# Kernel optimization log

Hardware: AMD Instinct MI355X
Metric: run time of the kernel (lower is better)

Reference implementation:

```python
import jax, jax.numpy as jnp
import numpy as np

D_IN = 1024
D_OUT = 1024
NUM_HEADS = 16
HEAD_DIM = D_OUT // NUM_HEADS


def setup_inputs() -> dict:
    key = jax.random.key(0)
    k_x, k_q, k_k, k_v, k_o, k_ob = jax.random.split(key, 6)
    s_in = 1.0 / np.sqrt(D_IN)
    s_out = 1.0 / np.sqrt(D_OUT)
    return {
        "x": jax.random.normal(k_x, (2, 2048, D_IN), dtype=jnp.float32),
        "W_q": jax.random.uniform(k_q, (D_IN, D_OUT), minval=-s_in, maxval=s_in, dtype=jnp.float32),
        "W_k": jax.random.uniform(k_k, (D_IN, D_OUT), minval=-s_in, maxval=s_in, dtype=jnp.float32),
        "W_v": jax.random.uniform(k_v, (D_IN, D_OUT), minval=-s_in, maxval=s_in, dtype=jnp.float32),
        "W_out": jax.random.uniform(k_o, (D_OUT, D_OUT), minval=-s_out, maxval=s_out, dtype=jnp.float32),
        "b_out": jax.random.uniform(k_ob, (D_OUT,), minval=-s_out, maxval=s_out, dtype=jnp.float32),
    }


def reference(x, W_q, W_k, W_v, W_out, b_out):
    b, t, _ = x.shape
    # projections (qkv_bias=False)
    q = (x @ W_q).reshape(b, t, NUM_HEADS, HEAD_DIM).transpose(0, 2, 1, 3)  # [b,h,t,d]
    k = (x @ W_k).reshape(b, t, NUM_HEADS, HEAD_DIM).transpose(0, 2, 1, 3)
    v = (x @ W_v).reshape(b, t, NUM_HEADS, HEAD_DIM).transpose(0, 2, 1, 3)
    scale = 1.0 / np.sqrt(HEAD_DIM).astype(np.float32)
    scores = jnp.einsum("bhqd,bhkd->bhqk", q, k) * scale  # [b,h,t,t]
    causal = jnp.triu(jnp.ones((t, t), dtype=bool), k=1)
    scores = jnp.where(causal, -jnp.inf, scores)
    weights = jax.nn.softmax(scores, axis=-1)
    # dropout p=0.0 -> identity
    context = jnp.einsum("bhqk,bhkd->bhqd", weights, v)
    context = context.transpose(0, 2, 1, 3).reshape(b, t, D_OUT)
    return context @ W_out + b_out
```

## Files before the change

kernel.cpp:

```cpp
#include <hip/hip_runtime.h>
#include <hip/hip_bf16.h>

#define B_  2
#define T_  2048
#define D_  1024
#define H_  16
#define DH_ 64
#define M_  (B_*T_)

typedef _Float16 f16;
typedef __attribute__((ext_vector_type(4))) _Float16 f16x4;
typedef __attribute__((ext_vector_type(8))) _Float16 f16x8;
typedef __attribute__((ext_vector_type(4))) float f32x4;

#define GLOAD_LDS(gp, lp) __builtin_amdgcn_global_load_lds( \
    (const __attribute__((address_space(1))) void*)(gp),    \
    (__attribute__((address_space(3))) void*)(lp), 16, 0, 0)

__global__ void prep(const float* __restrict__ x,
                     const float* __restrict__ wq, const float* __restrict__ wk,
                     const float* __restrict__ wv, const float* __restrict__ wo,
                     f16* __restrict__ xb, f16* __restrict__ wqkvT, f16* __restrict__ woutT) {
  __shared__ float tile[32][33];
  const int bid = blockIdx.x;
  if (bid < 2048) {
    size_t i = ((size_t)bid * 256 + threadIdx.x) * 8;
    float4 a = *(const float4*)(x + i);
    float4 b = *(const float4*)(x + i + 4);
    f16x8 o;
    o[0]=(f16)a.x; o[1]=(f16)a.y; o[2]=(f16)a.z; o[3]=(f16)a.w;
    o[4]=(f16)b.x; o[5]=(f16)b.y; o[6]=(f16)b.z; o[7]=(f16)b.w;
    *(f16x8*)(xb + i) = o;
  } else {
    const int b2 = bid - 2048;
    const int j = b2 >> 10, rem = b2 & 1023;
    const float* src = (j==0)?wq:(j==1)?wk:(j==2)?wv:wo;
    f16* dst = (j<3) ? (wqkvT + (size_t)j*D_*D_) : woutT;
    const int n0 = (rem & 31)*32, k0 = (rem >> 5)*32;
    const int tx = threadIdx.x & 31, ty = threadIdx.x >> 5;
    #pragma unroll
    for (int i=0;i<32;i+=8)
      tile[ty+i][tx] = src[(size_t)(k0+ty+i)*D_ + n0+tx];
    __syncthreads();
    #pragma unroll
    for (int i=0;i<32;i+=8)
      dst[(size_t)(n0+ty+i)*D_ + k0+tx] = (f16)tile[tx][ty+i];
  }
}

__launch_bounds__(256, 2)
__global__ void qkv_gemm(const f16* __restrict__ xb, const f16* __restrict__ wT,
                         f16* __restrict__ Qp, f16* __restrict__ Kp, f16* __restrict__ Vtp) {
  const int fid = blockIdx.x;
  const int g = fid & 7, r = fid >> 3;
  const int m0 = ((((r & 3) << 3) | g)) * 128;
  const int n0 = ((r >> 2) & 7) * 128;
  const int j  = r >> 5;
  const f16* B0 = wT + (size_t)j * D_ * D_;
  __shared__ alignas(16) char smem[65536];
  f16* AsF = (f16*)smem;
  f16* BsF = AsF + 2*128*64;
  const int tid = threadIdx.x;
  const int lane = tid & 63, wave = tid >> 6;
  const int ln = lane & 15, quad = lane >> 4;
  const int wm = wave >> 1, wn = wave & 1;

  f32x4 acc[4][4];
  #pragma unroll
  for (int a=0;a<4;++a)
    #pragma unroll
    for (int b=0;b<4;++b) acc[a][b] = f32x4{0.f,0.f,0.f,0.f};

  const bool swapped = (j < 2);
  const int slot_row[4] = { (0*256+tid)>>3, (1*256+tid)>>3, (2*256+tid)>>3, (3*256+tid)>>3 };

  #pragma unroll
  for (int p = 0; p < 4; ++p) {
    int slot = p*256 + tid;
    int row  = slot_row[p];
    int c    = (slot & 7) ^ (row & 7);
    GLOAD_LDS(xb + (size_t)(m0+row)*D_ + c*8, AsF + (size_t)slot*8);
    GLOAD_LDS(B0 + (size_t)(n0+row)*D_ + c*8, BsF + (size_t)slot*8);
  }
  __syncthreads();

  for (int it = 0; it < 16; ++it) {
    const f16* Ac = AsF + (it & 1)*8192;
    const f16* Bc = BsF + (it & 1)*8192;
    if (it < 15) {
      const int k1 = (it + 1) * 64;
      f16* An = AsF + ((it + 1) & 1)*8192;
      f16* Bn = BsF + ((it + 1) & 1)*8192;
      #pragma unroll
      for (int p = 0; p < 4; ++p) {
        int slot = p*256 + tid;
        int row  = slot_row[p];
        int c    = (slot & 7) ^ (row & 7);
        GLOAD_LDS(xb + (size_t)(m0+row)*D_ + k1 + c*8, An + (size_t)slot*8);
        GLOAD_LDS(B0 + (size_t)(n0+row)*D_ + k1 + c*8, Bn + (size_t)slot*8);
      }
    }
    #pragma unroll
    for (int ks = 0; ks < 2; ++ks) {
      const int cb = ((ks*4 + quad) ^ (ln & 7)) * 8;
      f16x8 af[4], bf[4];
      #pragma unroll
      for (int mt = 0; mt < 4; ++mt)
        af[mt] = *(const f16x8*)(Ac + (size_t)(wm*64 + mt*16 + ln)*64 + cb);
      #pragma unroll
      for (int nt = 0; nt < 4; ++nt)
        bf[nt] = *(const f16x8*)(Bc + (size_t)(wn*64 + nt*16 + ln)*64 + cb);
      if (swapped) {
        #pragma unroll
        for (int nt = 0; nt < 4; ++nt)
          #pragma unroll
          for (int mt = 0; mt < 4; ++mt)
            acc[nt][mt] = __builtin_amdgcn_mfma_f32_16x16x32_f16(bf[nt], af[mt], acc[nt][mt], 0, 0, 0);
      } else {
        #pragma unroll
        for (int mt = 0; mt < 4; ++mt)
          #pragma unroll
          for (int nt = 0; nt < 4; ++nt)
            acc[mt][nt] = __builtin_amdgcn_mfma_f32_16x16x32_f16(af[mt], bf[nt], acc[mt][nt], 0, 0, 0);
      }
    }
    __syncthreads();
  }

  if (swapped) {
    const float scale = (j == 0) ? 0.125f : 1.0f;
    f16* dstB = (j == 0) ? Qp : Kp;
    #pragma unroll
    for (int nt = 0; nt < 4; ++nt)
      #pragma unroll
      for (int mt = 0; mt < 4; ++mt) {
        int gm = m0 + wm*64 + mt*16 + ln;
        int gn = n0 + wn*64 + nt*16 + quad*4;
        int bb = gm >> 11, t = gm & (T_-1);
        int h  = gn >> 6,  dd = gn & (DH_-1);
        f16x4 v;
        #pragma unroll
        for (int rr = 0; rr < 4; ++rr) v[rr] = (f16)(acc[nt][mt][rr] * scale);
        *(f16x4*)&dstB[((((size_t)bb*H_ + h)*T_ + t)*DH_) + dd] = v;
      }
  } else {
    f16* VtS = (f16*)smem;
    #pragma unroll
    for (int mt = 0; mt < 4; ++mt)
      #pragma unroll
      for (int nt = 0; nt < 4; ++nt) {
        f16x4 v;
        v[0]=(f16)acc[mt][nt][0]; v[1]=(f16)acc[mt][nt][1];
        v[2]=(f16)acc[mt][nt][2]; v[3]=(f16)acc[mt][nt][3];
        *(f16x4*)&VtS[(size_t)(wn*64 + nt*16 + ln)*136 + wm*64 + mt*16 + quad*4] = v;
      }
    __syncthreads();
    int dd_loc = tid >> 1, half = tid & 1;
    int gn = n0 + dd_loc, h = gn >> 6, dd = gn & (DH_-1);
    int bb = m0 >> 11, tb = (m0 & (T_-1)) + half*64;
    f16* dst = Vtp + ((size_t)(bb*H_ + h)*DH_ + dd)*T_ + tb;
    const f16* src = VtS + (size_t)dd_loc*136 + half*64;
    #pragma unroll
    for (int u = 0; u < 8; ++u)
      *(uint4*)(dst + u*8) = *(const uint4*)(src + u*8);
  }
}

__launch_bounds__(256, 3)
__global__ void flash(const f16* __restrict__ Qp, const f16* __restrict__ Kp,
                      const f16* __restrict__ Vtp, f16* __restrict__ ctx) {
  const int fid = blockIdx.x;
  const int bh = fid & 31;
  const int qt = 31 - (fid >> 5);
  const int b = bh >> 4, h = bh & (H_-1);
  const f16* Kh = Kp  + (size_t)bh * T_ * DH_;
  const f16* Vh = Vtp + (size_t)bh * DH_ * T_;
  const f16* Qh = Qp  + (size_t)bh * T_ * DH_;
  const int tid = threadIdx.x, lane = tid & 63, w = tid >> 6;
  const int ln = lane & 15, quad = lane >> 4;
  __shared__ alignas(16) f16 Ks[2*64*64];
  __shared__ alignas(16) f16 Vs[2*64*64];
  __shared__ alignas(16) f16 Ps[64][72];

  const int qw = qt*64 + w*16;

  f16x8 qf[2];
  #pragma unroll
  for (int ks = 0; ks < 2; ++ks)
    qf[ks] = *(const f16x8*)&Qh[(size_t)(qw + ln)*DH_ + ks*32 + quad*8];

  f32x4 o[4];
  #pragma unroll
  for (int dt = 0; dt < 4; ++dt) o[dt] = f32x4{0.f,0.f,0.f,0.f};
  float l_part = 0.f;

  #pragma unroll
  for (int i = 0; i < 2; ++i) {
    int row = w*16 + i*8 + (lane >> 3);
    int c   = (lane & 7) ^ (row & 7);
    GLOAD_LDS(Kh + (size_t)row*DH_ + c*8, Ks + (w*128 + i*64 + lane)*8);
    GLOAD_LDS(Vh + (size_t)row*T_  + c*8, Vs + (w*128 + i*64 + lane)*8);
  }
  __syncthreads();

  for (int it = 0; it <= qt; ++it) {
    const f16* Kc = Ks + (it & 1)*4096;
    const f16* Vc = Vs + (it & 1)*4096;
    if (it < qt) {
      const int kv1 = (it + 1)*64;
      f16* Kn = Ks + ((it + 1) & 1)*4096;
      f16* Vn = Vs + ((it + 1) & 1)*4096;
      #pragma unroll
      for (int i = 0; i < 2; ++i) {
        int row = w*16 + i*8 + (lane >> 3);
        int c   = (lane & 7) ^ (row & 7);
        GLOAD_LDS(Kh + (size_t)(kv1 + row)*DH_ + c*8, Kn + (w*128 + i*64 + lane)*8);
        GLOAD_LDS(Vh + (size_t)row*T_ + kv1 + c*8,    Vn + (w*128 + i*64 + lane)*8);
      }
    }

    f32x4 s[4];
    #pragma unroll
    for (int kt = 0; kt < 4; ++kt) s[kt] = f32x4{0.f,0.f,0.f,0.f};
    #pragma unroll
    for (int ks = 0; ks < 2; ++ks) {
      f16x8 kx[4];
      #pragma unroll
      for (int kt = 0; kt < 4; ++kt)
        kx[kt] = *(const f16x8*)(Kc + (size_t)(kt*16 + ln)*64 + (((ks*4 + quad) ^ (ln & 7))*8));
      #pragma unroll
      for (int kt = 0; kt < 4; ++kt)
        s[kt] = __builtin_amdgcn_mfma_f32_16x16x32_f16(kx[kt], qf[ks], s[kt], 0, 0, 0);
    }
    if (it == qt) {
      const int kv0 = it*64;
      #pragma unroll
      for (int kt = 0; kt < 4; ++kt)
        #pragma unroll
        for (int rr = 0; rr < 4; ++rr)
          if (kv0 + kt*16 + quad*4 + rr > qw + ln) s[kt][rr] = -INFINITY;
    }
    #pragma unroll
    for (int kt = 0; kt < 4; ++kt) {
      f16x4 pk;
      #pragma unroll
      for (int rr = 0; rr < 4; ++rr) {
        float pe = __expf(s[kt][rr]);
        l_part += pe;
        pk[rr] = (f16)pe;
      }
      *(f16x4*)&Ps[w*16 + ln][kt*16 + quad*4] = pk;
    }
    asm volatile("" ::: "memory");

    #pragma unroll
    for (int ks = 0; ks < 2; ++ks) {
      f16x8 px = *(const f16x8*)&Ps[w*16 + ln][ks*32 + quad*8];
      #pragma unroll
      for (int dt = 0; dt < 4; ++dt) {
        f16x8 vy = *(const f16x8*)(Vc + (size_t)(dt*16 + ln)*64 + (((ks*4 + quad) ^ (ln & 7))*8));
        o[dt] = __builtin_amdgcn_mfma_f32_16x16x32_f16(px, vy, o[dt], 0, 0, 0);
      }
    }
    __syncthreads();
  }

  float l = l_part;
  l += __shfl_xor(l, 16, 64);
  l += __shfl_xor(l, 32, 64);
  float inv = 1.0f / l;
  #pragma unroll
  for (int rr = 0; rr < 4; ++rr) {
    float linv = __shfl(inv, quad*4 + rr, 64);
    int t = qt*64 + w*16 + quad*4 + rr;
    #pragma unroll
    for (int dt = 0; dt < 4; ++dt)
      ctx[(size_t)(b*T_ + t)*D_ + h*DH_ + dt*16 + ln] = (f16)(o[dt][rr] * linv);
  }
}

__launch_bounds__(256, 2)
__global__ void out_gemm(const f16* __restrict__ ctx, const f16* __restrict__ woT,
                         const float* __restrict__ bo, float* __restrict__ out) {
  const int fid = blockIdx.x;
  const int g = fid & 7, r = fid >> 3;
  const int m0 = ((((r & 3) << 3) | g)) * 128;
  const int n0 = (r >> 2) * 128;
  __shared__ alignas(16) f16 smem[4*128*64];
  f16* AsF = smem;
  f16* BsF = AsF + 2*128*64;
  const int tid = threadIdx.x;
  const int lane = tid & 63, wave = tid >> 6;
  const int ln = lane & 15, quad = lane >> 4;
  const int wm = wave >> 1, wn = wave & 1;

  f32x4 acc[4][4];
  #pragma unroll
  for (int a=0;a<4;++a)
    #pragma unroll
    for (int b=0;b<4;++b) acc[a][b] = f32x4{0.f,0.f,0.f,0.f};

  #pragma unroll
  for (int p = 0; p < 4; ++p) {
    int slot = p*256 + tid;
    int row  = slot >> 3;
    int c    = (slot & 7) ^ (row & 7);
    GLOAD_LDS(ctx + (size_t)(m0+row)*D_ + c*8, AsF + (size_t)slot*8);
    GLOAD_LDS(woT + (size_t)(n0+row)*D_ + c*8, BsF + (size_t)slot*8);
  }
  __syncthreads();

  for (int it = 0; it < 16; ++it) {
    const f16* Ac = AsF + (it & 1)*8192;
    const f16* Bc = BsF + (it & 1)*8192;
    if (it < 15) {
      const int k1 = (it + 1) * 64;
      f16* An = AsF + ((it + 1) & 1)*8192;
      f16* Bn = BsF + ((it + 1) & 1)*8192;
      #pragma unroll
      for (int p = 0; p < 4; ++p) {
        int slot = p*256 + tid;
        int row  = slot >> 3;
        int c    = (slot & 7) ^ (row & 7);
        GLOAD_LDS(ctx + (size_t)(m0+row)*D_ + k1 + c*8, An + (size_t)slot*8);
        GLOAD_LDS(woT + (size_t)(n0+row)*D_ + k1 + c*8, Bn + (size_t)slot*8);
      }
    }
    #pragma unroll
    for (int ks = 0; ks < 2; ++ks) {
      const int cb = ((ks*4 + quad) ^ (ln & 7)) * 8;
      f16x8 af[4], bf[4];
      #pragma unroll
      for (int mt = 0; mt < 4; ++mt)
        af[mt] = *(const f16x8*)(Ac + (size_t)(wm*64 + mt*16 + ln)*64 + cb);
      #pragma unroll
      for (int nt = 0; nt < 4; ++nt)
        bf[nt] = *(const f16x8*)(Bc + (size_t)(wn*64 + nt*16 + ln)*64 + cb);
      #pragma unroll
      for (int nt = 0; nt < 4; ++nt)
        #pragma unroll
        for (int mt = 0; mt < 4; ++mt)
          acc[nt][mt] = __builtin_amdgcn_mfma_f32_16x16x32_f16(bf[nt], af[mt], acc[nt][mt], 0, 0, 0);
    }
    __syncthreads();
  }

  #pragma unroll
  for (int nt = 0; nt < 4; ++nt) {
    int gn = n0 + wn*64 + nt*16 + quad*4;
    float4 bv = *(const float4*)&bo[gn];
    #pragma unroll
    for (int mt = 0; mt < 4; ++mt) {
      int gm = m0 + wm*64 + mt*16 + ln;
      float4 v;
      v.x = acc[nt][mt][0] + bv.x;
      v.y = acc[nt][mt][1] + bv.y;
      v.z = acc[nt][mt][2] + bv.z;
      v.w = acc[nt][mt][3] + bv.w;
      *(float4*)&out[(size_t)gm*D_ + gn] = v;
    }
  }
}

extern "C" void kernel_launch(void* const* d_in, const int* in_sizes, int n_in,
                              void* d_out, int out_size, void* d_ws, size_t ws_size,
                              hipStream_t stream) {
  const float* x  = (const float*)d_in[0];
  const float* wq = (const float*)d_in[1];
  const float* wk = (const float*)d_in[2];
  const float* wv = (const float*)d_in[3];
  const float* wo = (const float*)d_in[4];
  const float* bo = (const float*)d_in[5];
  float* out = (float*)d_out;

  f16* ws    = (f16*)d_ws;
  f16* xb    = ws;
  f16* wqkvT = xb    + (size_t)M_*D_;
  f16* woutT = wqkvT + (size_t)3*D_*D_;
  f16* Qb    = woutT + (size_t)D_*D_;
  f16* Kb    = Qb    + (size_t)M_*D_;
  f16* Vb    = Kb    + (size_t)M_*D_;
  f16* ctx   = Vb    + (size_t)M_*D_;

  prep<<<6144, 256, 0, stream>>>(x, wq, wk, wv, wo, xb, wqkvT, woutT);
  qkv_gemm<<<768, 256, 0, stream>>>(xb, wqkvT, Qb, Kb, Vb);
  flash<<<1024, 256, 0, stream>>>(Qb, Kb, Vb, ctx);
  out_gemm<<<256, 256, 0, stream>>>(ctx, woutT, bo, out);
}
```

Baseline: 162.6 us.

## Single-buffer GEMMs for occupancy, 128-row flash tiles, smaller out_gemm tiles

```diff
diff --git a/kernel.cpp b/kernel.cpp
--- a/kernel.cpp
+++ b/kernel.cpp
@@ -48,7 +48,7 @@
   }
 }
 
-__launch_bounds__(256, 2)
+__launch_bounds__(256, 4)
 __global__ void qkv_gemm(const f16* __restrict__ xb, const f16* __restrict__ wT,
                          f16* __restrict__ Qp, f16* __restrict__ Kp, f16* __restrict__ Vtp) {
   const int fid = blockIdx.x;
@@ -57,9 +57,9 @@
   const int n0 = ((r >> 2) & 7) * 128;
   const int j  = r >> 5;
   const f16* B0 = wT + (size_t)j * D_ * D_;
-  __shared__ alignas(16) char smem[65536];
+  __shared__ alignas(16) char smem[34816];
   f16* AsF = (f16*)smem;
-  f16* BsF = AsF + 2*128*64;
+  f16* BsF = AsF + 128*64;
   const int tid = threadIdx.x;
   const int lane = tid & 63, wave = tid >> 6;
   const int ln = lane & 15, quad = lane >> 4;
@@ -72,44 +72,28 @@
     for (int b=0;b<4;++b) acc[a][b] = f32x4{0.f,0.f,0.f,0.f};
 
   const bool swapped = (j < 2);
-  const int slot_row[4] = { (0*256+tid)>>3, (1*256+tid)>>3, (2*256+tid)>>3, (3*256+tid)>>3 };
-
-  #pragma unroll
-  for (int p = 0; p < 4; ++p) {
-    int slot = p*256 + tid;
-    int row  = slot_row[p];
-    int c    = (slot & 7) ^ (row & 7);
-    GLOAD_LDS(xb + (size_t)(m0+row)*D_ + c*8, AsF + (size_t)slot*8);
-    GLOAD_LDS(B0 + (size_t)(n0+row)*D_ + c*8, BsF + (size_t)slot*8);
-  }
-  __syncthreads();
 
   for (int it = 0; it < 16; ++it) {
-    const f16* Ac = AsF + (it & 1)*8192;
-    const f16* Bc = BsF + (it & 1)*8192;
-    if (it < 15) {
-      const int k1 = (it + 1) * 64;
-      f16* An = AsF + ((it + 1) & 1)*8192;
-      f16* Bn = BsF + ((it + 1) & 1)*8192;
-      #pragma unroll
-      for (int p = 0; p < 4; ++p) {
-        int slot = p*256 + tid;
-        int row  = slot_row[p];
-        int c    = (slot & 7) ^ (row & 7);
-        GLOAD_LDS(xb + (size_t)(m0+row)*D_ + k1 + c*8, An + (size_t)slot*8);
-        GLOAD_LDS(B0 + (size_t)(n0+row)*D_ + k1 + c*8, Bn + (size_t)slot*8);
-      }
-    }
+    const int k0 = it * 64;
+    #pragma unroll
+    for (int p = 0; p < 4; ++p) {
+      int slot = p*256 + tid;
+      int row  = slot >> 3;
+      int c    = (slot & 7) ^ (row & 7);
+      GLOAD_LDS(xb + (size_t)(m0+row)*D_ + k0 + c*8, AsF + (size_t)slot*8);
+      GLOAD_LDS(B0 + (size_t)(n0+row)*D_ + k0 + c*8, BsF + (size_t)slot*8);
+    }
+    __syncthreads();
     #pragma unroll
     for (int ks = 0; ks < 2; ++ks) {
       const int cb = ((ks*4 + quad) ^ (ln & 7)) * 8;
       f16x8 af[4], bf[4];
       #pragma unroll
       for (int mt = 0; mt < 4; ++mt)
-        af[mt] = *(const f16x8*)(Ac + (size_t)(wm*64 + mt*16 + ln)*64 + cb);
+        af[mt] = *(const f16x8*)(AsF + (size_t)(wm*64 + mt*16 + ln)*64 + cb);
       #pragma unroll
       for (int nt = 0; nt < 4; ++nt)
-        bf[nt] = *(const f16x8*)(Bc + (size_t)(wn*64 + nt*16 + ln)*64 + cb);
+        bf[nt] = *(const f16x8*)(BsF + (size_t)(wn*64 + nt*16 + ln)*64 + cb);
       if (swapped) {
         #pragma unroll
         for (int nt = 0; nt < 4; ++nt)
@@ -166,12 +150,12 @@
   }
 }
 
-__launch_bounds__(256, 3)
+__launch_bounds__(512, 6)
 __global__ void flash(const f16* __restrict__ Qp, const f16* __restrict__ Kp,
                       const f16* __restrict__ Vtp, f16* __restrict__ ctx) {
   const int fid = blockIdx.x;
   const int bh = fid & 31;
-  const int qt = 31 - (fid >> 5);
+  const int qt = 15 - (fid >> 5);
   const int b = bh >> 4, h = bh & (H_-1);
   const f16* Kh = Kp  + (size_t)bh * T_ * DH_;
   const f16* Vh = Vtp + (size_t)bh * DH_ * T_;
@@ -180,9 +164,9 @@
   const int ln = lane & 15, quad = lane >> 4;
   __shared__ alignas(16) f16 Ks[2*64*64];
   __shared__ alignas(16) f16 Vs[2*64*64];
-  __shared__ alignas(16) f16 Ps[64][72];
-
-  const int qw = qt*64 + w*16;
+  __shared__ alignas(16) f16 Ps[128][72];
+
+  const int qw = qt*128 + w*16;
 
   f16x8 qf[2];
   #pragma unroll
@@ -194,72 +178,67 @@
   for (int dt = 0; dt < 4; ++dt) o[dt] = f32x4{0.f,0.f,0.f,0.f};
   float l_part = 0.f;
 
-  #pragma unroll
-  for (int i = 0; i < 2; ++i) {
-    int row = w*16 + i*8 + (lane >> 3);
-    int c   = (lane & 7) ^ (row & 7);
-    GLOAD_LDS(Kh + (size_t)row*DH_ + c*8, Ks + (w*128 + i*64 + lane)*8);
-    GLOAD_LDS(Vh + (size_t)row*T_  + c*8, Vs + (w*128 + i*64 + lane)*8);
-  }
+  const int srow = tid >> 3;
+  const int sc   = (tid & 7) ^ (srow & 7);
+  GLOAD_LDS(Kh + (size_t)srow*DH_ + sc*8, Ks + (size_t)tid*8);
+  GLOAD_LDS(Vh + (size_t)srow*T_  + sc*8, Vs + (size_t)tid*8);
   __syncthreads();
 
-  for (int it = 0; it <= qt; ++it) {
+  const int nkv = 2*qt + 2;
+  for (int it = 0; it < nkv; ++it) {
+    const int kv0 = it * 64;
     const f16* Kc = Ks + (it & 1)*4096;
     const f16* Vc = Vs + (it & 1)*4096;
-    if (it < qt) {
-      const int kv1 = (it + 1)*64;
+    if (it + 1 < nkv) {
+      const int kv1 = kv0 + 64;
       f16* Kn = Ks + ((it + 1) & 1)*4096;
       f16* Vn = Vs + ((it + 1) & 1)*4096;
-      #pragma unroll
-      for (int i = 0; i < 2; ++i) {
-        int row = w*16 + i*8 + (lane >> 3);
-        int c   = (lane & 7) ^ (row & 7);
-        GLOAD_LDS(Kh + (size_t)(kv1 + row)*DH_ + c*8, Kn + (w*128 + i*64 + lane)*8);
-        GLOAD_LDS(Vh + (size_t)row*T_ + kv1 + c*8,    Vn + (w*128 + i*64 + lane)*8);
-      }
-    }
-
-    f32x4 s[4];
-    #pragma unroll
-    for (int kt = 0; kt < 4; ++kt) s[kt] = f32x4{0.f,0.f,0.f,0.f};
-    #pragma unroll
-    for (int ks = 0; ks < 2; ++ks) {
-      f16x8 kx[4];
-      #pragma unroll
-      for (int kt = 0; kt < 4; ++kt)
-        kx[kt] = *(const f16x8*)(Kc + (size_t)(kt*16 + ln)*64 + (((ks*4 + quad) ^ (ln & 7))*8));
-      #pragma unroll
-      for (int kt = 0; kt < 4; ++kt)
-        s[kt] = __builtin_amdgcn_mfma_f32_16x16x32_f16(kx[kt], qf[ks], s[kt], 0, 0, 0);
-    }
-    if (it == qt) {
-      const int kv0 = it*64;
-      #pragma unroll
-      for (int kt = 0; kt < 4; ++kt)
-        #pragma unroll
-        for (int rr = 0; rr < 4; ++rr)
-          if (kv0 + kt*16 + quad*4 + rr > qw + ln) s[kt][rr] = -INFINITY;
-    }
-    #pragma unroll
-    for (int kt = 0; kt < 4; ++kt) {
-      f16x4 pk;
-      #pragma unroll
-      for (int rr = 0; rr < 4; ++rr) {
-        float pe = __expf(s[kt][rr]);
-        l_part += pe;
-        pk[rr] = (f16)pe;
-      }
-      *(f16x4*)&Ps[w*16 + ln][kt*16 + quad*4] = pk;
-    }
-    asm volatile("" ::: "memory");
-
-    #pragma unroll
-    for (int ks = 0; ks < 2; ++ks) {
-      f16x8 px = *(const f16x8*)&Ps[w*16 + ln][ks*32 + quad*8];
-      #pragma unroll
-      for (int dt = 0; dt < 4; ++dt) {
-        f16x8 vy = *(const f16x8*)(Vc + (size_t)(dt*16 + ln)*64 + (((ks*4 + quad) ^ (ln & 7))*8));
-        o[dt] = __builtin_amdgcn_mfma_f32_16x16x32_f16(px, vy, o[dt], 0, 0, 0);
+      GLOAD_LDS(Kh + (size_t)(kv1 + srow)*DH_ + sc*8, Kn + (size_t)tid*8);
+      GLOAD_LDS(Vh + (size_t)srow*T_ + kv1 + sc*8,    Vn + (size_t)tid*8);
+    }
+
+    if (kv0 <= qw + 15) {
+      f32x4 s[4];
+      #pragma unroll
+      for (int kt = 0; kt < 4; ++kt) s[kt] = f32x4{0.f,0.f,0.f,0.f};
+      #pragma unroll
+      for (int ks = 0; ks < 2; ++ks) {
+        f16x8 kx[4];
+        #pragma unroll
+        for (int kt = 0; kt < 4; ++kt)
+          kx[kt] = *(const f16x8*)(Kc + (size_t)(kt*16 + ln)*64 + (((ks*4 + quad) ^ (ln & 7))*8));
+        #pragma unroll
+        for (int kt = 0; kt < 4; ++kt)
+          s[kt] = __builtin_amdgcn_mfma_f32_16x16x32_f16(kx[kt], qf[ks], s[kt], 0, 0, 0);
+      }
+      if (kv0 + 63 > qw) {
+        #pragma unroll
+        for (int kt = 0; kt < 4; ++kt)
+          #pragma unroll
+          for (int rr = 0; rr < 4; ++rr)
+            if (kv0 + kt*16 + quad*4 + rr > qw + ln) s[kt][rr] = -INFINITY;
+      }
+      #pragma unroll
+      for (int kt = 0; kt < 4; ++kt) {
+        f16x4 pk;
+        #pragma unroll
+        for (int rr = 0; rr < 4; ++rr) {
+          float pe = __expf(s[kt][rr]);
+          l_part += pe;
+          pk[rr] = (f16)pe;
+        }
+        *(f16x4*)&Ps[w*16 + ln][kt*16 + quad*4] = pk;
+      }
+      asm volatile("" ::: "memory");
+
+      #pragma unroll
+      for (int ks = 0; ks < 2; ++ks) {
+        f16x8 px = *(const f16x8*)&Ps[w*16 + ln][ks*32 + quad*8];
+        #pragma unroll
+        for (int dt = 0; dt < 4; ++dt) {
+          f16x8 vy = *(const f16x8*)(Vc + (size_t)(dt*16 + ln)*64 + (((ks*4 + quad) ^ (ln & 7))*8));
+          o[dt] = __builtin_amdgcn_mfma_f32_16x16x32_f16(px, vy, o[dt], 0, 0, 0);
+        }
       }
     }
     __syncthreads();
@@ -272,74 +251,65 @@
   #pragma unroll
   for (int rr = 0; rr < 4; ++rr) {
     float linv = __shfl(inv, quad*4 + rr, 64);
-    int t = qt*64 + w*16 + quad*4 + rr;
+    int t = qw + quad*4 + rr;
     #pragma unroll
     for (int dt = 0; dt < 4; ++dt)
       ctx[(size_t)(b*T_ + t)*D_ + h*DH_ + dt*16 + ln] = (f16)(o[dt][rr] * linv);
   }
 }
 
-__launch_bounds__(256, 2)
+__launch_bounds__(256, 5)
 __global__ void out_gemm(const f16* __restrict__ ctx, const f16* __restrict__ woT,
                          const float* __restrict__ bo, float* __restrict__ out) {
   const int fid = blockIdx.x;
   const int g = fid & 7, r = fid >> 3;
-  const int m0 = ((((r & 3) << 3) | g)) * 128;
-  const int n0 = (r >> 2) * 128;
-  __shared__ alignas(16) f16 smem[4*128*64];
+  const int m0 = (((r & 7) << 3) | g) * 64;
+  const int n0 = (r >> 3) * 128;
+  __shared__ alignas(16) f16 smem[64*64 + 128*64];
   f16* AsF = smem;
-  f16* BsF = AsF + 2*128*64;
+  f16* BsF = AsF + 64*64;
   const int tid = threadIdx.x;
   const int lane = tid & 63, wave = tid >> 6;
   const int ln = lane & 15, quad = lane >> 4;
   const int wm = wave >> 1, wn = wave & 1;
 
-  f32x4 acc[4][4];
+  f32x4 acc[4][2];
   #pragma unroll
   for (int a=0;a<4;++a)
     #pragma unroll
-    for (int b=0;b<4;++b) acc[a][b] = f32x4{0.f,0.f,0.f,0.f};
-
-  #pragma unroll
-  for (int p = 0; p < 4; ++p) {
-    int slot = p*256 + tid;
-    int row  = slot >> 3;
-    int c    = (slot & 7) ^ (row & 7);
-    GLOAD_LDS(ctx + (size_t)(m0+row)*D_ + c*8, AsF + (size_t)slot*8);
-    GLOAD_LDS(woT + (size_t)(n0+row)*D_ + c*8, BsF + (size_t)slot*8);
-  }
-  __syncthreads();
+    for (int b=0;b<2;++b) acc[a][b] = f32x4{0.f,0.f,0.f,0.f};
 
   for (int it = 0; it < 16; ++it) {
-    const f16* Ac = AsF + (it & 1)*8192;
-    const f16* Bc = BsF + (it & 1)*8192;
-    if (it < 15) {
-      const int k1 = (it + 1) * 64;
-      f16* An = AsF + ((it + 1) & 1)*8192;
-      f16* Bn = BsF + ((it + 1) & 1)*8192;
-      #pragma unroll
-      for (int p = 0; p < 4; ++p) {
-        int slot = p*256 + tid;
-        int row  = slot >> 3;
-        int c    = (slot & 7) ^ (row & 7);
-        GLOAD_LDS(ctx + (size_t)(m0+row)*D_ + k1 + c*8, An + (size_t)slot*8);
-        GLOAD_LDS(woT + (size_t)(n0+row)*D_ + k1 + c*8, Bn + (size_t)slot*8);
-      }
-    }
+    const int k0 = it * 64;
+    #pragma unroll
+    for (int p = 0; p < 2; ++p) {
+      int slot = p*256 + tid;
+      int row  = slot >> 3;
+      int c    = (slot & 7) ^ (row & 7);
+      GLOAD_LDS(ctx + (size_t)(m0+row)*D_ + k0 + c*8, AsF + (size_t)slot*8);
+    }
+    #pragma unroll
+    for (int p = 0; p < 4; ++p) {
+      int slot = p*256 + tid;
+      int row  = slot >> 3;
+      int c    = (slot & 7) ^ (row & 7);
+      GLOAD_LDS(woT + (size_t)(n0+row)*D_ + k0 + c*8, BsF + (size_t)slot*8);
+    }
+    __syncthreads();
     #pragma unroll
     for (int ks = 0; ks < 2; ++ks) {
       const int cb = ((ks*4 + quad) ^ (ln & 7)) * 8;
-      f16x8 af[4], bf[4];
-      #pragma unroll
-      for (int mt = 0; mt < 4; ++mt)
-        af[mt] = *(const f16x8*)(Ac + (size_t)(wm*64 + mt*16 + ln)*64 + cb);
+      f16x8 af[2], bf[4];
+      #pragma unroll
+      for (int mt = 0; mt < 2; ++mt)
+        af[mt] = *(const f16x8*)(AsF + (size_t)(wm*32 + mt*16 + ln)*64 + cb);
       #pragma unroll
       for (int nt = 0; nt < 4; ++nt)
-        bf[nt] = *(const f16x8*)(Bc + (size_t)(wn*64 + nt*16 + ln)*64 + cb);
+        bf[nt] = *(const f16x8*)(BsF + (size_t)(wn*64 + nt*16 + ln)*64 + cb);
       #pragma unroll
       for (int nt = 0; nt < 4; ++nt)
         #pragma unroll
-        for (int mt = 0; mt < 4; ++mt)
+        for (int mt = 0; mt < 2; ++mt)
           acc[nt][mt] = __builtin_amdgcn_mfma_f32_16x16x32_f16(bf[nt], af[mt], acc[nt][mt], 0, 0, 0);
     }
     __syncthreads();
@@ -350,8 +320,8 @@
     int gn = n0 + wn*64 + nt*16 + quad*4;
     float4 bv = *(const float4*)&bo[gn];
     #pragma unroll
-    for (int mt = 0; mt < 4; ++mt) {
-      int gm = m0 + wm*64 + mt*16 + ln;
+    for (int mt = 0; mt < 2; ++mt) {
+      int gm = m0 + wm*32 + mt*16 + ln;
       float4 v;
       v.x = acc[nt][mt][0] + bv.x;
       v.y = acc[nt][mt][1] + bv.y;
@@ -384,6 +354,6 @@
 
   prep<<<6144, 256, 0, stream>>>(x, wq, wk, wv, wo, xb, wqkvT, woutT);
   qkv_gemm<<<768, 256, 0, stream>>>(xb, wqkvT, Qb, Kb, Vb);
-  flash<<<1024, 256, 0, stream>>>(Qb, Kb, Vb, ctx);
-  out_gemm<<<256, 256, 0, stream>>>(ctx, woutT, bo, out);
-}
+  flash<<<512, 512, 0, stream>>>(Qb, Kb, Vb, ctx);
+  out_gemm<<<512, 256, 0, stream>>>(ctx, woutT, bo, out);
+}
```

After: 351.8 us. 2.16x slower.
